# Optimization experiments

Hardware: AMD Instinct MI355X
Metric: run time of the kernel (lower is better)

The kernel has to match this reference:

```python
import jax, jax.numpy as jnp
import numpy as np
from jax import lax

B, TENC, TMEL = 32, 512, 400
E, H, A, P, M, F, K = 512, 512, 512, 256, 128, 32, 31


def setup_inputs() -> dict:
    key = jax.random.key(0)
    ks = jax.random.split(key, 20)
    def rn(i, shape, fan_in):
        return jax.random.normal(ks[i], shape, jnp.float32) / np.float32(np.sqrt(fan_in))
    return dict(
        enc_outputs=jax.random.normal(ks[0], (B, TENC, 2 * E), jnp.float32),
        mel_spec_true=jax.random.normal(ks[1], (B, TMEL, M), jnp.float32),
        text_lens=jax.random.randint(ks[2], (B,), 0, TENC),
        mel_spec_lens=jax.random.randint(ks[3], (B,), 0, TMEL),
        max_text_len=TENC,
        pre_w1=rn(4, (M, P), M), pre_w2=rn(5, (P, P), P),
        attn_wi=rn(6, (P + E, 3 * H), P + E), attn_wh=rn(7, (H, 3 * H), H),
        attn_bi=jnp.zeros((3 * H,), jnp.float32), attn_bh=jnp.zeros((3 * H,), jnp.float32),
        q_w=rn(8, (H, A), H), k_w=rn(9, (2 * E, A), 2 * E),
        score_w=rn(10, (A, 1), A), score_b=jnp.zeros((1,), jnp.float32),
        loc_conv_w=rn(11, (F, 2, K), 2 * K), loc_w=rn(12, (F, A), F), loc_b=jnp.zeros((A,), jnp.float32),
        out_wi=rn(13, (A + H, 3 * H), A + H), out_wh=rn(14, (H, 3 * H), H),
        out_bi=jnp.zeros((3 * H,), jnp.float32), out_bh=jnp.zeros((3 * H,), jnp.float32),
        dec_w=rn(15, (H + A, M), H + A), dec_b=jnp.zeros((M,), jnp.float32),
        gate_w=rn(16, (H + A, 1), H + A), gate_b=jnp.zeros((1,), jnp.float32),
    )


def _gru_step(x, h, wi, wh, bi, bh):
    # single-step torch nn.GRU cell; gate order r, z, n
    gi = x @ wi + bi
    gh = h @ wh + bh
    ir, iz, inn = jnp.split(gi, 3, axis=-1)
    hr, hz, hn = jnp.split(gh, 3, axis=-1)
    r = jax.nn.sigmoid(ir + hr)
    z = jax.nn.sigmoid(iz + hz)
    n = jnp.tanh(inn + r * hn)
    return (1.0 - z) * n + z * h


def reference(enc_outputs, mel_spec_true, text_lens, mel_spec_lens, max_text_len,
              pre_w1, pre_w2, attn_wi, attn_wh, attn_bi, attn_bh,
              q_w, k_w, score_w, score_b, loc_conv_w, loc_w, loc_b,
              out_wi, out_wh, out_bi, out_bh, dec_w, dec_b, gate_w, gate_b):
    Bsz, Tenc, _ = enc_outputs.shape
    Tmel = mel_spec_true.shape[1]
    Hd = attn_wh.shape[0]
    Ad = k_w.shape[1]
    pad = (loc_conv_w.shape[2] - 1) // 2

    keys_p = enc_outputs @ k_w                                # [B,Tenc,A]
    enc_mask = jnp.arange(Tenc)[None, :] > text_lens[:, None]  # True = masked (t > len)

    def prenet(x):  # dropout disabled for determinism
        return jax.nn.relu(jax.nn.relu(x @ pre_w1) @ pre_w2)

    dec_in0 = prenet(jnp.zeros((Bsz, mel_spec_true.shape[2]), enc_outputs.dtype))
    carry0 = (jnp.zeros((Bsz, Hd), jnp.float32), jnp.zeros((Bsz, Hd), jnp.float32),
              jnp.zeros((Bsz, Tenc), jnp.float32), jnp.zeros((Bsz, Tenc), jnp.float32),
              jnp.zeros((Bsz, Ad), jnp.float32), dec_in0)

    def step(carry, _):
        h_attn, h_out, att_w, att_cum, ctx, dec_in = carry
        h_attn = _gru_step(jnp.concatenate([dec_in, ctx], -1), h_attn, attn_wi, attn_wh, attn_bi, attn_bh)
        loc_in = jnp.stack([att_w, att_cum], axis=1)           # [B,2,Tenc]
        loc = lax.conv_general_dilated(loc_in, loc_conv_w, (1,), [(pad, pad)],
                                       dimension_numbers=('NCH', 'OIH', 'NCH'))  # [B,F,Tenc]
        loc = jnp.swapaxes(loc, 1, 2) @ loc_w + loc_b          # [B,Tenc,A]
        q = (h_attn @ q_w)[:, None, :]                         # [B,1,A]
        s = (jnp.tanh(q + keys_p + loc) @ score_w + score_b)[..., 0]  # [B,Tenc]
        s = jnp.where(enc_mask, -jnp.inf, s)
        att_w = jax.nn.softmax(s, axis=1)
        ctx = jnp.einsum('bt,bta->ba', att_w, keys_p)
        att_cum = att_cum + att_w
        h_out = _gru_step(jnp.concatenate([h_attn, ctx], -1), h_out, out_wi, out_wh, out_bi, out_bh)
        att_h = jnp.concatenate([h_out, ctx], -1)
        mel = att_h @ dec_w + dec_b                            # [B,M]
        stop = (att_h @ gate_w + gate_b)[:, 0]                 # [B]
        dec_in = prenet(mel)                                   # teacher_force_ratio = 0
        return (h_attn, h_out, att_w, att_cum, ctx, dec_in), (mel, stop, att_w)

    _, (mels, gates, attns) = lax.scan(step, carry0, None, length=Tmel)
    mels = jnp.swapaxes(mels, 0, 1)    # [B,Tmel,M]
    gates = jnp.swapaxes(gates, 0, 1)  # [B,Tmel]
    attns = jnp.swapaxes(attns, 0, 1)  # [B,Tmel,Tenc]
    mel_mask = jnp.arange(Tmel)[None, :] > mel_spec_lens[:, None]
    masked_mel = jnp.where(mel_mask[:, :, None], 0.0, mels)
    masked_gate = jnp.where(mel_mask, 1000.0, gates)
    return masked_mel, masked_gate, attns, mel_mask
```

## Files before the change

### kernel.cpp

```cpp
#include <hip/hip_runtime.h>
#include <hip/hip_fp16.h>
#include <math.h>

#define NBLK 256
#define NTHR 1024

__device__ __forceinline__ float fast_rcp(float x) {
#if __has_builtin(__builtin_amdgcn_rcpf)
  return __builtin_amdgcn_rcpf(x);
#else
  return 1.f / x;
#endif
}
__device__ __forceinline__ float fast_sigmoid(float x) { return fast_rcp(1.f + __expf(-x)); }
__device__ __forceinline__ float fast_tanh(float x) { return 1.f - 2.f * fast_rcp(1.f + __expf(2.f * x)); }

union HU2 { unsigned int u; __half2 h; };
union HU4 { uint4 u; __half2 h[4]; };
__device__ __forceinline__ float2 cvt2(unsigned int u) { HU2 t; t.u = u; return __half22float2(t.h); }

__device__ __forceinline__ void sta(float* p, float v) {
  __hip_atomic_store(p, v, __ATOMIC_RELAXED, __HIP_MEMORY_SCOPE_AGENT);
}
__device__ __forceinline__ float lda(const float* p) {
  return __hip_atomic_load(p, __ATOMIC_RELAXED, __HIP_MEMORY_SCOPE_AGENT);
}

struct Params {
  const float *enc, *pre_w1, *pre_w2, *attn_bi, *attn_bh;
  const float *q_w, *k_w, *score_w, *score_b, *conv_w, *loc_w, *loc_b;
  const float *out_bi, *out_bh, *dec_b, *gate_b;
  const float *attn_wi, *attn_wh, *out_wi, *out_wh, *dec_w, *gate_w;
  const int *text_lens, *mel_lens;
  __half *hkeys, *gw1T, *gw2T, *decT, *pre1T, *pre2T, *gateh, *locwh, *qwT;
  float *hA, *hO, *attw, *attcum, *decin, *ebuf, *zpart, *ctxacc, *stateZ;
  int *done;
  unsigned *barc;
  float *out_mel, *out_gate, *out_attn, *out_mask;
};

__device__ __forceinline__ void gbar(unsigned* flags, unsigned* gen, unsigned e,
                                     int blk, int tid) {
  __syncthreads();
  if (tid == 0) {
    asm volatile("s_waitcnt vmcnt(0) lgkmcnt(0)" ::: "memory");
    __hip_atomic_store(&flags[blk], e, __ATOMIC_RELAXED, __HIP_MEMORY_SCOPE_AGENT);
  }
  if (blk == 0) {
    if (tid < 64) {
      while (true) {
        bool ok = true;
#pragma unroll
        for (int j = 0; j < 4; j++) {
          unsigned v = __hip_atomic_load(&flags[tid * 4 + j], __ATOMIC_RELAXED,
                                         __HIP_MEMORY_SCOPE_AGENT);
          ok &= (v >= e);
        }
        if (__all(ok)) break;
        __builtin_amdgcn_s_sleep(1);
      }
      if (tid == 0)
        __hip_atomic_store(gen, e, __ATOMIC_RELAXED, __HIP_MEMORY_SCOPE_AGENT);
    }
  } else {
    if (tid == 0) {
      while (__hip_atomic_load(gen, __ATOMIC_RELAXED, __HIP_MEMORY_SCOPE_AGENT) < e)
        __builtin_amdgcn_s_sleep(2);
    }
  }
  asm volatile("" ::: "memory");
  __syncthreads();
}

__global__ __launch_bounds__(512) void k_keys(Params p) {
  __shared__ float sA[16][132];
  __shared__ float sB[16][68];
  int tid = threadIdx.x;
  int row0 = blockIdx.x * 128, col0 = blockIdx.y * 64;
  float acc[4][4] = {};
  int r = tid >> 2, kq = tid & 3;
  int tx = tid & 15, ty = tid >> 4;
  for (int k0 = 0; k0 < 1024; k0 += 16) {
    __syncthreads();
    float4 a4 = *(const float4*)(p.enc + (size_t)(row0 + r) * 1024 + k0 + kq * 4);
    sA[kq * 4 + 0][r] = a4.x; sA[kq * 4 + 1][r] = a4.y;
    sA[kq * 4 + 2][r] = a4.z; sA[kq * 4 + 3][r] = a4.w;
    if (tid < 256) {
      int kb = tid >> 4, nb = (tid & 15) * 4;
      float4 b4 = *(const float4*)(p.k_w + (size_t)(k0 + kb) * 512 + col0 + nb);
      sB[kb][nb + 0] = b4.x; sB[kb][nb + 1] = b4.y;
      sB[kb][nb + 2] = b4.z; sB[kb][nb + 3] = b4.w;
    }
    __syncthreads();
#pragma unroll
    for (int k = 0; k < 16; k++) {
      float ar[4], br[4];
#pragma unroll
      for (int i = 0; i < 4; i++) { ar[i] = sA[k][ty * 4 + i]; br[i] = sB[k][tx * 4 + i]; }
#pragma unroll
      for (int i = 0; i < 4; i++)
#pragma unroll
        for (int j = 0; j < 4; j++) acc[i][j] = fmaf(ar[i], br[j], acc[i][j]);
    }
  }
#pragma unroll
  for (int i = 0; i < 4; i++)
#pragma unroll
    for (int j = 0; j < 4; j++)
      p.hkeys[(size_t)(row0 + ty * 4 + i) * 512 + col0 + tx * 4 + j] = __float2half(acc[i][j]);
}

__global__ __launch_bounds__(256) void k_repack(Params p) {
  const int gsz = gridDim.x * 256;
  const int t0 = blockIdx.x * 256 + threadIdx.x;
  for (int i = t0; i < 1280 * 512; i += gsz) {
    int r = i >> 9, u = i & 511;
    const float* src = (r < 768) ? p.attn_wi + (size_t)r * 1536 : p.attn_wh + (size_t)(r - 768) * 1536;
    __half2* d = (__half2*)(p.gw1T + ((size_t)i << 2));
    d[0] = __halves2half2(__float2half(src[u]), __float2half(src[512 + u]));
    d[1] = __halves2half2(__float2half(src[1024 + u]), __float2half(0.f));
  }
  for (int i = t0; i < 1536 * 512; i += gsz) {
    int r = i >> 9, u = i & 511;
    const float* src = (r < 1024) ? p.out_wi + (size_t)r * 1536 : p.out_wh + (size_t)(r - 1024) * 1536;
    __half2* d = (__half2*)(p.gw2T + ((size_t)i << 2));
    d[0] = __halves2half2(__float2half(src[u]), __float2half(src[512 + u]));
    d[1] = __halves2half2(__float2half(src[1024 + u]), __float2half(0.f));
  }
  for (int i = t0; i < 512 * 512; i += gsz) {
    int k = i >> 9, a = i & 511;
    p.qwT[(size_t)a * 512 + k] = __float2half(p.q_w[(size_t)k * 512 + a]);
  }
  for (int i = t0; i < 1024 * 128; i += gsz) {
    int k = i >> 7, m = i & 127;
    p.decT[(size_t)m * 1024 + k] = __float2half(p.dec_w[(size_t)k * 128 + m]);
  }
  for (int i = t0; i < 1024; i += gsz) p.gateh[i] = __float2half(p.gate_w[i]);
  for (int i = t0; i < 16384; i += gsz) p.locwh[i] = __float2half(p.loc_w[i]);
  for (int i = t0; i < 128 * 256; i += gsz) {
    int m = i >> 8, pc = i & 255;
    p.pre1T[(size_t)pc * 128 + m] = __float2half(p.pre_w1[(size_t)m * 256 + pc]);
  }
  for (int i = t0; i < 256 * 256; i += gsz) {
    int k = i >> 8, pc = i & 255;
    p.pre2T[(size_t)pc * 256 + k] = __float2half(p.pre_w2[(size_t)k * 256 + pc]);
  }
  for (int i = t0; i < 106496; i += gsz) p.stateZ[i] = 0.f;
  for (int i = t0; i < 16384; i += gsz) p.ctxacc[i] = 0.f;
  for (int i = t0; i < 512; i += gsz) p.barc[i] = 0u;
  for (int i = t0; i < 32; i += gsz) p.done[i] = 0;
  for (int i = t0; i < 12800; i += gsz) {
    int b = i / 400, t = i - b * 400;
    p.out_mask[i] = (t > p.mel_lens[b]) ? 1.f : 0.f;
  }
}

struct SMemMega {
  __half keysL[64 * 512];
  float ctxL[4][512];
  float invZ[4];
  union {
    struct { float x[4][1536]; float4 part4[16][64]; } gr;
    struct { float locS[64][33]; float aw[94]; float ac[94]; float hA_s[512]; float qS[512];
             float qpart[2][512]; float cpred[8][512]; float eS[64]; } s3;
    struct { float xh[1024]; float red[1024]; float mel[128]; float p1[256]; } s6;
  } u;
};

template <int DXI, int RPK>
__device__ __forceinline__ void gru_compute(SMemMega& sm, const uint2* w512,
    const float* __restrict__ bi, const float* __restrict__ bh,
    float* __restrict__ hnext, int ug, int b0, int tid) {
  const int u = tid & 15, b2 = (tid >> 4) & 3, ks = tid >> 6;
  const int uG = (ug << 4) + u;
  float ar = 0.f, az = 0.f, ani = 0.f, anh = 0.f;
  const uint2* w = w512 + (size_t)(ks * RPK) * 512 + uG;
#pragma unroll 8
  for (int j = 0; j < RPK; j++) {
    uint2 wv = w[(size_t)j * 512];
    int r = ks * RPK + j;
    float x = sm.u.gr.x[b2][r];
    float2 f0 = cvt2(wv.x);
    float2 f1 = cvt2(wv.y);
    ar = fmaf(x, f0.x, ar);
    az = fmaf(x, f0.y, az);
    float t = x * f1.x;
    if (r < DXI) ani += t; else anh += t;
  }
  sm.u.gr.part4[ks][(u << 2) + b2] = make_float4(ar, az, ani, anh);
  __syncthreads();
  if (tid < 64) {
    int uu = tid >> 2, bb2 = tid & 3;
    float4 s = make_float4(0.f, 0.f, 0.f, 0.f);
#pragma unroll
    for (int l = 0; l < 16; l++) {
      float4 v = sm.u.gr.part4[l][(uu << 2) + bb2];
      s.x += v.x; s.y += v.y; s.z += v.z; s.w += v.w;
    }
    int uGf = (ug << 4) + uu;
    float r = fast_sigmoid(s.x + bi[uGf] + bh[uGf]);
    float z = fast_sigmoid(s.y + bi[512 + uGf] + bh[512 + uGf]);
    float n = fast_tanh(s.z + bi[1024 + uGf] + r * (s.w + bh[1024 + uGf]));
    float hv = sm.u.gr.x[bb2][DXI + uGf];
    sta(&hnext[((size_t)(b0 + bb2) << 9) + uGf], (1.f - z) * n + z * hv);
  }
}

__global__ __launch_bounds__(NTHR) void mega(Params p) {
  __shared__ SMemMega sm;
  const int blk = blockIdx.x, tid = threadIdx.x;
  const int ug = blk & 31, bg = blk >> 5, b0 = bg * 4;
  const int bS = blk & 31, t8 = blk >> 5, t0g = t8 << 6;
  unsigned epoch = 0;
  unsigned* flags = p.barc;
  unsigned* gen = p.barc + 384;

  {
    const uint4* src = (const uint4*)(p.hkeys + (((size_t)(bS << 9) + t0g) << 9));
    uint4* dst = (uint4*)sm.keysL;
    for (int i = tid; i < 4096; i += NTHR) dst[i] = src[i];
    for (int i = tid; i < 2048; i += NTHR) sm.ctxL[i >> 9][i & 511] = 0.f;
  }
  __syncthreads();

#pragma clang loop unroll(disable)
  for (int step = 0; step < 400; step++) {
    const int par = step & 1;
    float* hA_prev = p.hA + par * 16384;
    float* hA_next = p.hA + (par ^ 1) * 16384;
    float* hO_prev = p.hO + par * 16384;
    float* hO_next = p.hO + (par ^ 1) * 16384;

    {
      if (ug == 0) {
        for (int i = tid; i < 2048; i += NTHR)
          sta(&p.ctxacc[(b0 << 9) + i], 0.f);
      }
      for (int i = tid; i < 1024; i += NTHR) {
        int b2 = i >> 8, r = i & 255;
        sm.u.gr.x[b2][r] = lda(&p.decin[((b0 + b2) << 8) + r]);
      }
      for (int i = tid; i < 2048; i += NTHR) {
        int b2 = i >> 9, a = i & 511;
        sm.u.gr.x[b2][256 + a] = sm.ctxL[b2][a];
      }
      for (int i = tid; i < 2048; i += NTHR) {
        int b2 = i >> 9, a = i & 511;
        sm.u.gr.x[b2][768 + a] = lda(&hA_prev[((b0 + b2) << 9) + a]);
      }
      __syncthreads();
      gru_compute<768, 80>(sm, (const uint2*)p.gw1T, p.attn_bi, p.attn_bh,
                           hA_next, ug, b0, tid);
    }
    gbar(flags, gen, ++epoch, blk, tid);

    {
      const int tlen = p.text_lens[bS];
      for (int j = tid; j < 94; j += NTHR) {
        int pp = t0g - 15 + j;
        bool ok = (unsigned)pp < 512u;
        sm.u.s3.aw[j] = ok ? lda(&p.attw[(bS << 9) + pp]) : 0.f;
        sm.u.s3.ac[j] = ok ? lda(&p.attcum[(bS << 9) + pp]) : 0.f;
      }
      if (tid < 512) sm.u.s3.hA_s[tid] = lda(&hA_next[(bS << 9) + tid]);
      __syncthreads();
      for (int i = tid; i < 2048; i += NTHR) {
        int tt = i >> 5, f = i & 31;
        const float* w0 = p.conv_w + f * 62;
        float a = 0.f;
#pragma unroll
        for (int k = 0; k < 31; k++)
          a = fmaf(w0[k], sm.u.s3.aw[tt + k], fmaf(w0[31 + k], sm.u.s3.ac[tt + k], a));
        sm.u.s3.locS[tt][f] = a;
      }
      {
        int a = tid & 511, ks = tid >> 9;
        const HU4* qp = (const HU4*)(p.qwT + (size_t)a * 512 + ks * 256);
        float q0 = 0.f, q1 = 0.f;
#pragma unroll 4
        for (int it = 0; it < 32; it++) {
          HU4 raw = qp[it];
          int kb = ks * 256 + it * 8;
#pragma unroll
          for (int h2 = 0; h2 < 4; h2++) {
            float2 w = __half22float2(raw.h[h2]);
            q0 = fmaf(sm.u.s3.hA_s[kb + h2 * 2], w.x, q0);
            q1 = fmaf(sm.u.s3.hA_s[kb + h2 * 2 + 1], w.y, q1);
          }
        }
        sm.u.s3.qpart[ks][a] = q0 + q1;
      }
      __syncthreads();
      if (tid < 512)
        sm.u.s3.qS[tid] = sm.u.s3.qpart[0][tid] + sm.u.s3.qpart[1][tid] + p.loc_b[tid];
      __syncthreads();
      const int lane = tid & 63, wv = tid >> 6;
      float acc[4][8];
      float4 qA = *(const float4*)&sm.u.s3.qS[lane * 8];
      float4 qB = *(const float4*)&sm.u.s3.qS[lane * 8 + 4];
#pragma unroll
      for (int j = 0; j < 4; j++) {
        int tL = wv * 4 + j;
        HU4 raw; raw.u = *(const uint4*)&sm.keysL[tL * 512 + lane * 8];
        float2 k0 = __half22float2(raw.h[0]), k1 = __half22float2(raw.h[1]);
        float2 k2 = __half22float2(raw.h[2]), k3 = __half22float2(raw.h[3]);
        acc[j][0] = qA.x + k0.x; acc[j][1] = qA.y + k0.y;
        acc[j][2] = qA.z + k1.x; acc[j][3] = qA.w + k1.y;
        acc[j][4] = qB.x + k2.x; acc[j][5] = qB.y + k2.y;
        acc[j][6] = qB.z + k3.x; acc[j][7] = qB.w + k3.y;
      }
#pragma unroll 4
      for (int f = 0; f < 32; f++) {
        HU4 rw; rw.u = *(const uint4*)(p.locwh + (size_t)f * 512 + lane * 8);
        float2 w0 = __half22float2(rw.h[0]), w1 = __half22float2(rw.h[1]);
        float2 w2 = __half22float2(rw.h[2]), w3 = __half22float2(rw.h[3]);
#pragma unroll
        for (int j = 0; j < 4; j++) {
          float lf = sm.u.s3.locS[wv * 4 + j][f];
          acc[j][0] = fmaf(lf, w0.x, acc[j][0]); acc[j][1] = fmaf(lf, w0.y, acc[j][1]);
          acc[j][2] = fmaf(lf, w1.x, acc[j][2]); acc[j][3] = fmaf(lf, w1.y, acc[j][3]);
          acc[j][4] = fmaf(lf, w2.x, acc[j][4]); acc[j][5] = fmaf(lf, w2.y, acc[j][5]);
          acc[j][6] = fmaf(lf, w3.x, acc[j][6]); acc[j][7] = fmaf(lf, w3.y, acc[j][7]);
        }
      }
      float4 sA = *(const float4*)(p.score_w + lane * 8);
      float4 sB = *(const float4*)(p.score_w + lane * 8 + 4);
      float sbias = p.score_b[0];
      float e_reg[4];
#pragma unroll
      for (int j = 0; j < 4; j++) {
        float pv = fast_tanh(acc[j][0]) * sA.x + fast_tanh(acc[j][1]) * sA.y +
                   fast_tanh(acc[j][2]) * sA.z + fast_tanh(acc[j][3]) * sA.w +
                   fast_tanh(acc[j][4]) * sB.x + fast_tanh(acc[j][5]) * sB.y +
                   fast_tanh(acc[j][6]) * sB.z + fast_tanh(acc[j][7]) * sB.w;
#pragma unroll
        for (int off = 32; off > 0; off >>= 1) pv += __shfl_xor(pv, off, 64);
        int t = t0g + wv * 4 + j;
        e_reg[j] = (t > tlen) ? 0.f : __expf(pv + sbias);
      }
      if (lane == 0) {
#pragma unroll
        for (int j = 0; j < 4; j++) sm.u.s3.eS[wv * 4 + j] = e_reg[j];
      }
      float cp[8] = {0.f, 0.f, 0.f, 0.f, 0.f, 0.f, 0.f, 0.f};
#pragma unroll
      for (int j = 0; j < 4; j++) {
        int tL = wv * 4 + j;
        HU4 raw; raw.u = *(const uint4*)&sm.keysL[tL * 512 + lane * 8];
        float2 k0 = __half22float2(raw.h[0]), k1 = __half22float2(raw.h[1]);
        float2 k2 = __half22float2(raw.h[2]), k3 = __half22float2(raw.h[3]);
        float e = e_reg[j];
        cp[0] = fmaf(e, k0.x, cp[0]); cp[1] = fmaf(e, k0.y, cp[1]);
        cp[2] = fmaf(e, k1.x, cp[2]); cp[3] = fmaf(e, k1.y, cp[3]);
        cp[4] = fmaf(e, k2.x, cp[4]); cp[5] = fmaf(e, k2.y, cp[5]);
        cp[6] = fmaf(e, k3.x, cp[6]); cp[7] = fmaf(e, k3.y, cp[7]);
      }
      __syncthreads();
      if (wv < 8) {
        float4* r0 = (float4*)&sm.u.s3.cpred[wv][lane * 8];
        r0[0] = make_float4(cp[0], cp[1], cp[2], cp[3]);
        r0[1] = make_float4(cp[4], cp[5], cp[6], cp[7]);
      }
      __syncthreads();
      if (wv >= 8) {
        float* r0 = &sm.u.s3.cpred[wv - 8][lane * 8];
#pragma unroll
        for (int i = 0; i < 8; i++) r0[i] += cp[i];
      }
      __syncthreads();
      if (tid < 512) {
        float s = 0.f;
#pragma unroll
        for (int j = 0; j < 8; j++) s += sm.u.s3.cpred[j][tid];
        atomicAdd(&p.ctxacc[(bS << 9) + tid], s);
      }
      if (tid < 64) {
        float e = sm.u.s3.eS[tid];
        sta(&p.ebuf[(bS << 9) + t0g + tid], e);
        float z = e;
#pragma unroll
        for (int off = 32; off > 0; off >>= 1) z += __shfl_xor(z, off, 64);
        if (tid == 0) sta(&p.zpart[bS * 8 + t8], z);
      }
    }
    gbar(flags, gen, ++epoch, blk, tid);

    {
      if (tid < 4) {
        float Z = 0.f;
#pragma unroll
        for (int j = 0; j < 8; j++) Z += lda(&p.zpart[(b0 + tid) * 8 + j]);
        sm.invZ[tid] = fast_rcp(Z);
      }
      __syncthreads();
      for (int i = tid; i < 2048; i += NTHR) {
        int b2 = i >> 9, a = i & 511;
        sm.ctxL[b2][a] = lda(&p.ctxacc[((b0 + b2) << 9) + a]) * sm.invZ[b2];
      }
      if (ug == 0) {
        for (int i = tid; i < 2048; i += NTHR) {
          int b2 = i >> 9, t = i & 511;
          int bb = b0 + b2;
          float v = lda(&p.ebuf[(bb << 9) + t]) * sm.invZ[b2];
          sta(&p.attw[(bb << 9) + t], v);
          float oc = lda(&p.attcum[(bb << 9) + t]);
          sta(&p.attcum[(bb << 9) + t], oc + v);
          p.out_attn[(size_t)bb * 204800 + (size_t)step * 512 + t] = v;
        }
      }
      __syncthreads();
      for (int i = tid; i < 2048; i += NTHR) {
        int b2 = i >> 9, a = i & 511;
        sm.u.gr.x[b2][a] = lda(&hA_next[((b0 + b2) << 9) + a]);
      }
      for (int i = tid; i < 2048; i += NTHR) {
        int b2 = i >> 9, a = i & 511;
        sm.u.gr.x[b2][512 + a] = sm.ctxL[b2][a];
      }
      for (int i = tid; i < 2048; i += NTHR) {
        int b2 = i >> 9, a = i & 511;
        sm.u.gr.x[b2][1024 + a] = lda(&hO_prev[((b0 + b2) << 9) + a]);
      }
      __syncthreads();
      gru_compute<1024, 96>(sm, (const uint2*)p.gw2T, p.out_bi, p.out_bh,
                            hO_next, ug, b0, tid);
      asm volatile("s_waitcnt vmcnt(0)" ::: "memory");
      __syncthreads();
      if (tid < 4) atomicAdd(&p.done[b0 + tid], 1);
      if (ug < 4) {
        const int bb = b0 + ug;
        if (tid == 0) {
          int target = 32 * (step + 1);
          while (__hip_atomic_load(&p.done[bb], __ATOMIC_RELAXED,
                                   __HIP_MEMORY_SCOPE_AGENT) < target)
            __builtin_amdgcn_s_sleep(2);
        }
        __syncthreads();
        sm.u.s6.xh[tid] = (tid < 512) ? lda(&hO_next[(bb << 9) + tid])
                                      : sm.ctxL[ug][tid - 512];
        __syncthreads();
        bool masked = step > p.mel_lens[bb];
        {
          int m = tid & 127, ks = tid >> 7;
          const HU4* dp = (const HU4*)(p.decT + (size_t)m * 1024 + ks * 128);
          float a = 0.f;
#pragma unroll 4
          for (int it = 0; it < 16; it++) {
            HU4 raw = dp[it];
            int kb = ks * 128 + it * 8;
#pragma unroll
            for (int h2 = 0; h2 < 4; h2++) {
              float2 w = __half22float2(raw.h[h2]);
              a = fmaf(sm.u.s6.xh[kb + h2 * 2], w.x, a);
              a = fmaf(sm.u.s6.xh[kb + h2 * 2 + 1], w.y, a);
            }
          }
          sm.u.s6.red[tid] = a;
        }
        __syncthreads();
        if (tid < 128) {
          float mv = p.dec_b[tid];
#pragma unroll
          for (int j = 0; j < 8; j++) mv += sm.u.s6.red[tid + j * 128];
          sm.u.s6.mel[tid] = mv;
          p.out_mel[(size_t)bb * 51200 + (size_t)step * 128 + tid] = masked ? 0.f : mv;
        }
        __syncthreads();
        sm.u.s6.red[tid] = sm.u.s6.xh[tid] * __half2float(p.gateh[tid]);
        __syncthreads();
        if (tid < 64) {
          float g = 0.f;
#pragma unroll
          for (int j = 0; j < 16; j++) g += sm.u.s6.red[tid + j * 64];
#pragma unroll
          for (int off = 32; off > 0; off >>= 1) g += __shfl_xor(g, off, 64);
          if (tid == 0) p.out_gate[bb * 400 + step] = masked ? 1000.f : (g + p.gate_b[0]);
        }
        __syncthreads();
        {
          int pc = tid & 255, ks = tid >> 8;
          const HU4* wp = (const HU4*)(p.pre1T + (size_t)pc * 128 + ks * 32);
          float a = 0.f;
#pragma unroll
          for (int it = 0; it < 4; it++) {
            HU4 raw = wp[it];
            int kb = ks * 32 + it * 8;
#pragma unroll
            for (int h2 = 0; h2 < 4; h2++) {
              float2 w = __half22float2(raw.h[h2]);
              a = fmaf(sm.u.s6.mel[kb + h2 * 2], w.x, a);
              a = fmaf(sm.u.s6.mel[kb + h2 * 2 + 1], w.y, a);
            }
          }
          sm.u.s6.red[tid] = a;
        }
        __syncthreads();
        if (tid < 256) {
          float a = sm.u.s6.red[tid] + sm.u.s6.red[tid + 256] +
                    sm.u.s6.red[tid + 512] + sm.u.s6.red[tid + 768];
          sm.u.s6.p1[tid] = fmaxf(a, 0.f);
        }
        __syncthreads();
        {
          int pc = tid & 255, ks = tid >> 8;
          const HU4* wp = (const HU4*)(p.pre2T + (size_t)pc * 256 + ks * 64);
          float a = 0.f;
#pragma unroll
          for (int it = 0; it < 8; it++) {
            HU4 raw = wp[it];
            int kb = ks * 64 + it * 8;
#pragma unroll
            for (int h2 = 0; h2 < 4; h2++) {
              float2 w = __half22float2(raw.h[h2]);
              a = fmaf(sm.u.s6.p1[kb + h2 * 2], w.x, a);
              a = fmaf(sm.u.s6.p1[kb + h2 * 2 + 1], w.y, a);
            }
          }
          sm.u.s6.red[tid] = a;
        }
        __syncthreads();
        if (tid < 256) {
          float a = sm.u.s6.red[tid] + sm.u.s6.red[tid + 256] +
                    sm.u.s6.red[tid + 512] + sm.u.s6.red[tid + 768];
          sta(&p.decin[(bb << 8) + tid], fmaxf(a, 0.f));
        }
      }
    }
    gbar(flags, gen, ++epoch, blk, tid);
  }
}

extern "C" void kernel_launch(void* const* d_in, const int* in_sizes, int n_in,
                              void* d_out, int out_size, void* d_ws, size_t ws_size,
                              hipStream_t stream) {
  Params p;
  p.enc       = (const float*)d_in[0];
  p.text_lens = (const int*)d_in[2];
  p.mel_lens  = (const int*)d_in[3];
  p.pre_w1    = (const float*)d_in[5];
  p.pre_w2    = (const float*)d_in[6];
  p.attn_wi   = (const float*)d_in[7];
  p.attn_wh   = (const float*)d_in[8];
  p.attn_bi   = (const float*)d_in[9];
  p.attn_bh   = (const float*)d_in[10];
  p.q_w       = (const float*)d_in[11];
  p.k_w       = (const float*)d_in[12];
  p.score_w   = (const float*)d_in[13];
  p.score_b   = (const float*)d_in[14];
  p.conv_w    = (const float*)d_in[15];
  p.loc_w     = (const float*)d_in[16];
  p.loc_b     = (const float*)d_in[17];
  p.out_wi    = (const float*)d_in[18];
  p.out_wh    = (const float*)d_in[19];
  p.out_bi    = (const float*)d_in[20];
  p.out_bh    = (const float*)d_in[21];
  p.dec_w     = (const float*)d_in[22];
  p.dec_b     = (const float*)d_in[23];
  p.gate_w    = (const float*)d_in[24];
  p.gate_b    = (const float*)d_in[25];

  float* ws = (float*)d_ws;
  p.hkeys  = (__half*)(ws);
  p.gw1T   = (__half*)(ws + 4194304);
  p.gw2T   = (__half*)(ws + 5505024);
  p.decT   = (__half*)(ws + 7077888);
  p.pre1T  = (__half*)(ws + 7143424);
  p.pre2T  = (__half*)(ws + 7159808);
  p.gateh  = (__half*)(ws + 7192576);
  p.locwh  = (__half*)(ws + 7193088);
  p.qwT    = (__half*)(ws + 7201280);
  p.hA     = ws + 7332352;
  p.hO     = ws + 7365120;
  p.attw   = ws + 7397888;
  p.attcum = ws + 7414272;
  p.decin  = ws + 7430656;
  p.stateZ = p.hA;
  p.ebuf   = ws + 7438848;
  p.zpart  = ws + 7455232;
  p.ctxacc = ws + 7455488;
  p.done   = (int*)(ws + 7471872);
  p.barc   = (unsigned*)(ws + 7471904);
  float* out = (float*)d_out;
  p.out_mel  = out;
  p.out_gate = out + 1638400;
  p.out_attn = out + 1651200;
  p.out_mask = out + 8204800;

  k_repack<<<2048, 256, 0, stream>>>(p);
  k_keys<<<dim3(128, 8), 512, 0, stream>>>(p);
  void* args[] = { (void*)&p };
  hipLaunchCooperativeKernel((const void*)mega, dim3(NBLK), dim3(NTHR), args, 0, stream);
}
```

Measured before the change: 41.05 ms.

## Precompute next-step attention GRU partial sums early and prefetch weights into cache

```diff
diff --git a/kernel.cpp b/kernel.cpp
--- a/kernel.cpp
+++ b/kernel.cpp
@@ -25,6 +25,7 @@
 __device__ __forceinline__ float lda(const float* p) {
   return __hip_atomic_load(p, __ATOMIC_RELAXED, __HIP_MEMORY_SCOPE_AGENT);
 }
+__device__ __forceinline__ void ntst(float* p, float v) { __builtin_nontemporal_store(v, p); }
 
 struct Params {
   const float *enc, *pre_w1, *pre_w2, *attn_bi, *attn_bh;
@@ -65,7 +66,7 @@
   } else {
     if (tid == 0) {
       while (__hip_atomic_load(gen, __ATOMIC_RELAXED, __HIP_MEMORY_SCOPE_AGENT) < e)
-        __builtin_amdgcn_s_sleep(2);
+        __builtin_amdgcn_s_sleep(1);
     }
   }
   asm volatile("" ::: "memory");
@@ -160,49 +161,26 @@
   float ctxL[4][512];
   float invZ[4];
   union {
-    struct { float x[4][1536]; float4 part4[16][64]; } gr;
+    struct { float x[4][1544]; float4 part4[16][64]; } gr;
     struct { float locS[64][33]; float aw[94]; float ac[94]; float hA_s[512]; float qS[512];
              float qpart[2][512]; float cpred[8][512]; float eS[64]; } s3;
     struct { float xh[1024]; float red[1024]; float mel[128]; float p1[256]; } s6;
   } u;
 };
 
-template <int DXI, int RPK>
-__device__ __forceinline__ void gru_compute(SMemMega& sm, const uint2* w512,
-    const float* __restrict__ bi, const float* __restrict__ bh,
-    float* __restrict__ hnext, int ug, int b0, int tid) {
-  const int u = tid & 15, b2 = (tid >> 4) & 3, ks = tid >> 6;
-  const int uG = (ug << 4) + u;
-  float ar = 0.f, az = 0.f, ani = 0.f, anh = 0.f;
-  const uint2* w = w512 + (size_t)(ks * RPK) * 512 + uG;
+__device__ __forceinline__ void gchunk(const uint2* __restrict__ w,
+                                       const float* __restrict__ x, int ks,
+                                       int j0, int j1,
+                                       float& a0, float& a1, float& a2) {
 #pragma unroll 8
-  for (int j = 0; j < RPK; j++) {
-    uint2 wv = w[(size_t)j * 512];
-    int r = ks * RPK + j;
-    float x = sm.u.gr.x[b2][r];
+  for (int j = j0; j < j1; ++j) {
+    uint2 wv = w[(size_t)j << 13];
+    float xv = x[ks + (j << 4)];
     float2 f0 = cvt2(wv.x);
-    float2 f1 = cvt2(wv.y);
-    ar = fmaf(x, f0.x, ar);
-    az = fmaf(x, f0.y, az);
-    float t = x * f1.x;
-    if (r < DXI) ani += t; else anh += t;
-  }
-  sm.u.gr.part4[ks][(u << 2) + b2] = make_float4(ar, az, ani, anh);
-  __syncthreads();
-  if (tid < 64) {
-    int uu = tid >> 2, bb2 = tid & 3;
-    float4 s = make_float4(0.f, 0.f, 0.f, 0.f);
-#pragma unroll
-    for (int l = 0; l < 16; l++) {
-      float4 v = sm.u.gr.part4[l][(uu << 2) + bb2];
-      s.x += v.x; s.y += v.y; s.z += v.z; s.w += v.w;
-    }
-    int uGf = (ug << 4) + uu;
-    float r = fast_sigmoid(s.x + bi[uGf] + bh[uGf]);
-    float z = fast_sigmoid(s.y + bi[512 + uGf] + bh[512 + uGf]);
-    float n = fast_tanh(s.z + bi[1024 + uGf] + r * (s.w + bh[1024 + uGf]));
-    float hv = sm.u.gr.x[bb2][DXI + uGf];
-    sta(&hnext[((size_t)(b0 + bb2) << 9) + uGf], (1.f - z) * n + z * hv);
+    float nf = cvt2(wv.y).x;
+    a0 = fmaf(xv, f0.x, a0);
+    a1 = fmaf(xv, f0.y, a1);
+    a2 = fmaf(xv, nf, a2);
   }
 }
 
@@ -215,6 +193,11 @@
   unsigned* flags = p.barc;
   unsigned* gen = p.barc + 384;
 
+  const int u_ = tid & 15, b2_ = (tid >> 4) & 3, ks_ = tid >> 6;
+  const int uG_ = (ug << 4) + u_;
+  const uint2* w1 = (const uint2*)p.gw1T + ((size_t)ks_ << 9) + uG_;
+  const uint2* w2 = (const uint2*)p.gw2T + ((size_t)ks_ << 9) + uG_;
+
   {
     const uint4* src = (const uint4*)(p.hkeys + (((size_t)(bS << 9) + t0g) << 9));
     uint4* dst = (uint4*)sm.keysL;
@@ -222,6 +205,8 @@
     for (int i = tid; i < 2048; i += NTHR) sm.ctxL[i >> 9][i & 511] = 0.f;
   }
   __syncthreads();
+
+  float g1r = 0.f, g1z = 0.f, g1ni = 0.f, g1nh = 0.f;
 
 #pragma clang loop unroll(disable)
   for (int step = 0; step < 400; step++) {
@@ -232,29 +217,60 @@
     float* hO_next = p.hO + (par ^ 1) * 16384;
 
     {
+      float pq0, pq1, pq2, pq3, pq4 = 0.f;
+      {
+        const float* qw = (const float*)p.qwT;
+        pq0 = qw[(size_t)tid << 5];
+        pq1 = qw[((size_t)tid + 1024) << 5];
+        pq2 = qw[((size_t)tid + 2048) << 5];
+        pq3 = qw[((size_t)tid + 3072) << 5];
+        if (tid < 256) pq4 = ((const float*)p.locwh)[(size_t)tid << 5];
+      }
       if (ug == 0) {
         for (int i = tid; i < 2048; i += NTHR)
           sta(&p.ctxacc[(b0 << 9) + i], 0.f);
       }
-      for (int i = tid; i < 1024; i += NTHR) {
-        int b2 = i >> 8, r = i & 255;
-        sm.u.gr.x[b2][r] = lda(&p.decin[((b0 + b2) << 8) + r]);
-      }
-      for (int i = tid; i < 2048; i += NTHR) {
-        int b2 = i >> 9, a = i & 511;
-        sm.u.gr.x[b2][256 + a] = sm.ctxL[b2][a];
-      }
-      for (int i = tid; i < 2048; i += NTHR) {
-        int b2 = i >> 9, a = i & 511;
-        sm.u.gr.x[b2][768 + a] = lda(&hA_prev[((b0 + b2) << 9) + a]);
-      }
-      __syncthreads();
-      gru_compute<768, 80>(sm, (const uint2*)p.gw1T, p.attn_bi, p.attn_bh,
-                           hA_next, ug, b0, tid);
+      for (int i = tid; i < 1024; i += NTHR)
+        sm.u.gr.x[i >> 8][i & 255] = lda(&p.decin[((b0 + (i >> 8)) << 8) + (i & 255)]);
+      __syncthreads();
+      gchunk(w1, &sm.u.gr.x[b2_][0], ks_, 0, 16, g1r, g1z, g1ni);
+      sm.u.gr.part4[ks_][(u_ << 2) + b2_] = make_float4(g1r, g1z, g1ni, g1nh);
+      __syncthreads();
+      if (tid < 64) {
+        int uu = tid >> 2, bb2 = tid & 3;
+        float4 s = make_float4(0.f, 0.f, 0.f, 0.f);
+#pragma unroll
+        for (int l = 0; l < 16; l++) {
+          float4 v = sm.u.gr.part4[l][(uu << 2) + bb2];
+          s.x += v.x; s.y += v.y; s.z += v.z; s.w += v.w;
+        }
+        int uGf = (ug << 4) + uu;
+        float r = fast_sigmoid(s.x + p.attn_bi[uGf] + p.attn_bh[uGf]);
+        float z = fast_sigmoid(s.y + p.attn_bi[512 + uGf] + p.attn_bh[512 + uGf]);
+        float n = fast_tanh(s.z + p.attn_bi[1024 + uGf] + r * (s.w + p.attn_bh[1024 + uGf]));
+        float hv = lda(&hA_prev[((b0 + bb2) << 9) + uGf]);
+        sta(&hA_next[((b0 + bb2) << 9) + uGf], (1.f - z) * n + z * hv);
+      }
+      asm volatile("" :: "v"(pq0), "v"(pq1), "v"(pq2), "v"(pq3), "v"(pq4));
     }
     gbar(flags, gen, ++epoch, blk, tid);
 
     {
+      float pf0, pf1 = 0.f, pf2, pf3 = 0.f, pf4 = 0.f, pf5 = 0.f;
+      {
+        const float* g1 = (const float*)p.gw1T + (ug << 5);
+        const float* g2 = (const float*)p.gw2T + (ug << 5);
+        pf0 = g1[(size_t)tid << 10];
+        if (tid < 256) pf1 = g1[((size_t)tid + 1024) << 10];
+        pf2 = g2[(size_t)tid << 10];
+        if (tid < 512) pf3 = g2[((size_t)tid + 1024) << 10];
+        if (ug < 4) {
+          const float* dt = (const float*)p.decT;
+          pf4 = dt[(size_t)tid << 5] + dt[((size_t)tid + 1024) << 5];
+          if (tid < 512) pf5 = ((const float*)p.pre1T)[(size_t)tid << 5];
+          pf5 += ((const float*)p.pre2T)[(size_t)tid << 5];
+        }
+      }
       const int tlen = p.text_lens[bS];
       for (int j = tid; j < 94; j += NTHR) {
         int pp = t0g - 15 + j;
@@ -382,6 +398,7 @@
         for (int off = 32; off > 0; off >>= 1) z += __shfl_xor(z, off, 64);
         if (tid == 0) sta(&p.zpart[bS * 8 + t8], z);
       }
+      asm volatile("" :: "v"(pf0), "v"(pf1), "v"(pf2), "v"(pf3), "v"(pf4), "v"(pf5));
     }
     gbar(flags, gen, ++epoch, blk, tid);
 
@@ -405,7 +422,7 @@
           sta(&p.attw[(bb << 9) + t], v);
           float oc = lda(&p.attcum[(bb << 9) + t]);
           sta(&p.attcum[(bb << 9) + t], oc + v);
-          p.out_attn[(size_t)bb * 204800 + (size_t)step * 512 + t] = v;
+          ntst(&p.out_attn[(size_t)bb * 204800 + (size_t)step * 512 + t], v);
         }
       }
       __syncthreads();
@@ -422,18 +439,43 @@
         sm.u.gr.x[b2][1024 + a] = lda(&hO_prev[((b0 + b2) << 9) + a]);
       }
       __syncthreads();
-      gru_compute<1024, 96>(sm, (const uint2*)p.gw2T, p.out_bi, p.out_bh,
-                            hO_next, ug, b0, tid);
+      {
+        float r2 = 0.f, z2 = 0.f, ni2 = 0.f, nh2 = 0.f;
+        gchunk(w2, &sm.u.gr.x[b2_][0], ks_, 0, 64, r2, z2, ni2);
+        gchunk(w2, &sm.u.gr.x[b2_][0], ks_, 64, 96, r2, z2, nh2);
+        sm.u.gr.part4[ks_][(u_ << 2) + b2_] = make_float4(r2, z2, ni2, nh2);
+      }
+      __syncthreads();
+      if (tid < 64) {
+        int uu = tid >> 2, bb2 = tid & 3;
+        float4 s = make_float4(0.f, 0.f, 0.f, 0.f);
+#pragma unroll
+        for (int l = 0; l < 16; l++) {
+          float4 v = sm.u.gr.part4[l][(uu << 2) + bb2];
+          s.x += v.x; s.y += v.y; s.z += v.z; s.w += v.w;
+        }
+        int uGf = (ug << 4) + uu;
+        float r = fast_sigmoid(s.x + p.out_bi[uGf] + p.out_bh[uGf]);
+        float z = fast_sigmoid(s.y + p.out_bi[512 + uGf] + p.out_bh[512 + uGf]);
+        float n = fast_tanh(s.z + p.out_bi[1024 + uGf] + r * (s.w + p.out_bh[1024 + uGf]));
+        float hv = sm.u.gr.x[bb2][1024 + uGf];
+        sta(&hO_next[((b0 + bb2) << 9) + uGf], (1.f - z) * n + z * hv);
+      }
       asm volatile("s_waitcnt vmcnt(0)" ::: "memory");
       __syncthreads();
       if (tid < 4) atomicAdd(&p.done[b0 + tid], 1);
+      g1r = 0.f; g1z = 0.f; g1ni = 0.f; g1nh = 0.f;
+      if (step < 399) {
+        gchunk(w1, &sm.u.gr.x[b2_][0] + 256, ks_, 16, 48, g1r, g1z, g1ni);
+        gchunk(w1, &sm.u.gr.x[b2_][0] - 768, ks_, 48, 80, g1r, g1z, g1nh);
+      }
       if (ug < 4) {
         const int bb = b0 + ug;
         if (tid == 0) {
           int target = 32 * (step + 1);
           while (__hip_atomic_load(&p.done[bb], __ATOMIC_RELAXED,
                                    __HIP_MEMORY_SCOPE_AGENT) < target)
-            __builtin_amdgcn_s_sleep(2);
+            __builtin_amdgcn_s_sleep(1);
         }
         __syncthreads();
         sm.u.s6.xh[tid] = (tid < 512) ? lda(&hO_next[(bb << 9) + tid])
@@ -463,7 +505,7 @@
 #pragma unroll
           for (int j = 0; j < 8; j++) mv += sm.u.s6.red[tid + j * 128];
           sm.u.s6.mel[tid] = mv;
-          p.out_mel[(size_t)bb * 51200 + (size_t)step * 128 + tid] = masked ? 0.f : mv;
+          ntst(&p.out_mel[(size_t)bb * 51200 + (size_t)step * 128 + tid], masked ? 0.f : mv);
         }
         __syncthreads();
         sm.u.s6.red[tid] = sm.u.s6.xh[tid] * __half2float(p.gateh[tid]);
@@ -474,7 +516,7 @@
           for (int j = 0; j < 16; j++) g += sm.u.s6.red[tid + j * 64];
 #pragma unroll
           for (int off = 32; off > 0; off >>= 1) g += __shfl_xor(g, off, 64);
-          if (tid == 0) p.out_gate[bb * 400 + step] = masked ? 1000.f : (g + p.gate_b[0]);
+          if (tid == 0) ntst(&p.out_gate[bb * 400 + step], masked ? 1000.f : (g + p.gate_b[0]));
         }
         __syncthreads();
         {
```

After: 48.09 ms. 1.17x slower.
